# Optimization experiments

Measured on AMD Instinct MI355X. Metric: run time of the kernel, lower is better.

The kernel has to match this reference:

```python
import jax, jax.numpy as jnp
import numpy as np

N_NODES = 50000
N_EDGES = 800000
N_FEAT = 64
N_LAYERS = 3


def setup_inputs() -> dict:
    key = jax.random.key(0)
    k1, k2, k3 = jax.random.split(key, 3)
    x = jax.random.normal(k1, (N_NODES, N_FEAT), dtype=jnp.float32)
    edge_index = jax.random.randint(k2, (2, N_EDGES), 0, N_NODES, dtype=jnp.int64)
    # num_layers Linear(F, F, bias=False) weights; torch init U(-1/sqrt(F), 1/sqrt(F))
    bound = 1.0 / np.sqrt(N_FEAT)
    weights = jax.random.uniform(k3, (N_LAYERS, N_FEAT, N_FEAT), dtype=jnp.float32,
                                 minval=-bound, maxval=bound)
    return {"x": x, "edge_index": edge_index, "weights": weights}


def reference(x, edge_index, weights):
    n = x.shape[0]
    # self_loop=True: add_self_loops appends (i, i) for every node
    self_idx = jnp.arange(n, dtype=edge_index.dtype)
    src = jnp.concatenate([edge_index[0], self_idx])
    dst = jnp.concatenate([edge_index[1], self_idx])
    # in-degree for mean aggregation (>=1 thanks to self loops)
    deg = jax.ops.segment_sum(jnp.ones(src.shape[0], dtype=x.dtype), dst,
                              num_segments=n)
    inv_deg = (1.0 / jnp.maximum(deg, 1.0))[:, None]  # [N,1]
    for l in range(weights.shape[0]):
        # scatter-mean: gather source features, sum at target, divide by degree
        agg = jax.ops.segment_sum(x[src], dst, num_segments=n) * inv_deg  # [N,F]
        # Linear(bias=False): agg @ W.T
        x = agg @ weights[l].T
    return x
```

## Files before the change

### kernel.cpp

```cpp
#include <hip/hip_runtime.h>

#define NN 50000
#define NE 800000
#define NF 64
#define NL 3

typedef unsigned int uint;
typedef unsigned short ushort;
using short8 = __attribute__((ext_vector_type(8))) short;
using f32x4  = __attribute__((ext_vector_type(4))) float;

__device__ inline ushort f2bf(float f) {
    uint u = __float_as_uint(f);
    u += 0x7fffu + ((u >> 16) & 1u);
    return (ushort)(u >> 16);
}
__device__ inline float bf2f(ushort h) { return __uint_as_float(((uint)h) << 16); }


__global__ void zero_k(int* __restrict__ p, int n) {
    int i = blockIdx.x * blockDim.x + threadIdx.x;
    if (i < n) p[i] = 0;
}

__global__ void fill_k(const int* __restrict__ src, const int* __restrict__ dst,
                       int* __restrict__ deg, int* __restrict__ colp, int e) {
    int i = blockIdx.x * blockDim.x + threadIdx.x;
    if (i < e) {
        int d = dst[i];
        int slot = atomicAdd(&deg[d], 1);
        if (slot < 64) colp[(size_t)d * 64 + slot] = src[i];
    }
}

__global__ __launch_bounds__(256) void gather_k(const float* __restrict__ x,
                                                const int* __restrict__ deg,
                                                const int* __restrict__ colp,
                                                float* __restrict__ agg, int n) {
    int tid = threadIdx.x;
    int lane = tid & 63;
    int row = blockIdx.x * 4 + (tid >> 6);
    if (row >= n) return;
    int dg = deg[row];
    float invd = 1.0f / (float)(dg + 1);
    const int* cp = colp + (size_t)row * 64;
    float acc0 = x[(size_t)row * NF + lane];
    float acc1 = 0.f, acc2 = 0.f, acc3 = 0.f;
    int e = 0;
    for (; e + 8 <= dg; e += 8) {
        int4 ca = ((const int4*)cp)[(e >> 2)];
        int4 cb = ((const int4*)cp)[(e >> 2) + 1];
        float v0 = x[(size_t)ca.x * NF + lane];
        float v1 = x[(size_t)ca.y * NF + lane];
        float v2 = x[(size_t)ca.z * NF + lane];
        float v3 = x[(size_t)ca.w * NF + lane];
        float v4 = x[(size_t)cb.x * NF + lane];
        float v5 = x[(size_t)cb.y * NF + lane];
        float v6 = x[(size_t)cb.z * NF + lane];
        float v7 = x[(size_t)cb.w * NF + lane];
        acc0 += v0; acc1 += v1; acc2 += v2; acc3 += v3;
        acc0 += v4; acc1 += v5; acc2 += v6; acc3 += v7;
    }
    for (; e < dg; ++e)
        acc0 += x[(size_t)cp[e] * NF + lane];
    agg[(size_t)row * NF + lane] = (acc0 + acc1 + acc2 + acc3) * invd;
}

__global__ __launch_bounds__(256) void gemm_k(const float* __restrict__ A,
                                              const float* __restrict__ Wg,
                                              float* __restrict__ O, int n) {
    int tid = threadIdx.x;
    int lane = tid & 63, w = tid >> 6;
    int m = lane & 15, g = lane >> 4;
    int ko = g * 8;
    int row0 = blockIdx.x * 64;

    int arow = row0 + w * 16 + m;
    if (arow > n - 1) arow = n - 1;
    const float* ar = A + (size_t)arow * NF;

    float af[16];
    *(float4*)(af + 0)  = *(const float4*)(ar + ko);
    *(float4*)(af + 4)  = *(const float4*)(ar + ko + 4);
    *(float4*)(af + 8)  = *(const float4*)(ar + 32 + ko);
    *(float4*)(af + 12) = *(const float4*)(ar + 32 + ko + 4);

    short8 ah0, al0, ah1, al1;
    #pragma unroll
    for (int i = 0; i < 8; ++i) {
        ushort h = f2bf(af[i]);
        ah0[i] = (short)h; al0[i] = (short)f2bf(af[i] - bf2f(h));
        ushort h2 = f2bf(af[8 + i]);
        ah1[i] = (short)h2; al1[i] = (short)f2bf(af[8 + i] - bf2f(h2));
    }

    f32x4 acc[4];
    #pragma unroll
    for (int t = 0; t < 4; ++t) {
        const float* wr = Wg + (size_t)(t * 16 + m) * NF;
        float wf[16];
        *(float4*)(wf + 0)  = *(const float4*)(wr + ko);
        *(float4*)(wf + 4)  = *(const float4*)(wr + ko + 4);
        *(float4*)(wf + 8)  = *(const float4*)(wr + 32 + ko);
        *(float4*)(wf + 12) = *(const float4*)(wr + 32 + ko + 4);
        short8 bh0, bl0, bh1, bl1;
        #pragma unroll
        for (int i = 0; i < 8; ++i) {
            ushort h = f2bf(wf[i]);
            bh0[i] = (short)h; bl0[i] = (short)f2bf(wf[i] - bf2f(h));
            ushort h2 = f2bf(wf[8 + i]);
            bh1[i] = (short)h2; bl1[i] = (short)f2bf(wf[8 + i] - bf2f(h2));
        }
        f32x4 c = {0.f, 0.f, 0.f, 0.f};
        c = __builtin_amdgcn_mfma_f32_16x16x32_bf16(ah0, bh0, c, 0, 0, 0);
        c = __builtin_amdgcn_mfma_f32_16x16x32_bf16(ah1, bh1, c, 0, 0, 0);
        c = __builtin_amdgcn_mfma_f32_16x16x32_bf16(al0, bh0, c, 0, 0, 0);
        c = __builtin_amdgcn_mfma_f32_16x16x32_bf16(al1, bh1, c, 0, 0, 0);
        c = __builtin_amdgcn_mfma_f32_16x16x32_bf16(ah0, bl0, c, 0, 0, 0);
        c = __builtin_amdgcn_mfma_f32_16x16x32_bf16(ah1, bl1, c, 0, 0, 0);
        acc[t] = c;
    }

    #pragma unroll
    for (int t = 0; t < 4; ++t) {
        #pragma unroll
        for (int r = 0; r < 4; ++r) {
            int orow = row0 + w * 16 + g * 4 + r;
            if (orow < n) O[(size_t)orow * NF + t * 16 + m] = acc[t][r];
        }
    }
}

extern "C" void kernel_launch(void* const* d_in, const int* in_sizes, int n_in,
                              void* d_out, int out_size, void* d_ws, size_t ws_size,
                              hipStream_t stream) {
    const float* x_in = (const float*)d_in[0];
    const int*   edge = (const int*)d_in[1];
    const float* Wg   = (const float*)d_in[2];
    float* out = (float*)d_out;

    int*   deg  = (int*)d_ws;
    int*   colp = (int*)((char*)d_ws + (256 << 10));
    float* agg  = (float*)((char*)d_ws + (14 << 20));

    zero_k<<<(NN + 255) / 256, 256, 0, stream>>>(deg, NN);
    fill_k<<<(NE + 255) / 256, 256, 0, stream>>>(edge, edge + NE, deg, colp, NE);

    const int gb = (NN + 3) / 4;
    const int mb = (NN + 63) / 64;

    gather_k<<<gb, 256, 0, stream>>>(x_in, deg, colp, agg, NN);
    gemm_k  <<<mb, 256, 0, stream>>>(agg, Wg + 0 * NF * NF, out, NN);
    gather_k<<<gb, 256, 0, stream>>>(out, deg, colp, agg, NN);
    gemm_k  <<<mb, 256, 0, stream>>>(agg, Wg + 1 * NF * NF, out, NN);
    gather_k<<<gb, 256, 0, stream>>>(out, deg, colp, agg, NN);
    gemm_k  <<<mb, 256, 0, stream>>>(agg, Wg + 2 * NF * NF, out, NN);
}
```

Measured before the change: 268.6 us.

## Fuse neighbor gather with MFMA linear per layer and slice CSR fill by destination

Gather-mean and the split-bf16 MFMA linear are merged into one kernel per layer. Each block aggregates 64 rows into shared memory and multiplies them by W directly, so the agg array never goes out to global memory and back, and three launches are dropped. The fill kernel now partitions destinations into 8 slices per block group, aiming for more local atomics and colp writes. The costs are that every edge is re-read 8 times, and each block now gathers 64 rows with only 4 waves and 64-row blocks, which may reduce the latency hiding in the gather.

Result: slower. 320.9 us (+19.5%).

```diff
diff --git a/kernel.cpp b/kernel.cpp
--- a/kernel.cpp
+++ b/kernel.cpp
@@ -4,6 +4,9 @@
 #define NE 800000
 #define NF 64
 #define NL 3
+#define PAD 64
+#define NSLICE 8
+#define SLICE_N ((NN + NSLICE - 1) / NSLICE)
 
 typedef unsigned int uint;
 typedef unsigned short ushort;
@@ -17,67 +20,73 @@
 }
 __device__ inline float bf2f(ushort h) { return __uint_as_float(((uint)h) << 16); }
 
-
 __global__ void zero_k(int* __restrict__ p, int n) {
     int i = blockIdx.x * blockDim.x + threadIdx.x;
     if (i < n) p[i] = 0;
 }
 
-__global__ void fill_k(const int* __restrict__ src, const int* __restrict__ dst,
-                       int* __restrict__ deg, int* __restrict__ colp, int e) {
-    int i = blockIdx.x * blockDim.x + threadIdx.x;
-    if (i < e) {
+__global__ void fill_sliced_k(const int* __restrict__ src, const int* __restrict__ dst,
+                              int* __restrict__ deg, int* __restrict__ colp, int e) {
+    int slice = blockIdx.x & (NSLICE - 1);
+    int chunk = blockIdx.x >> 3;
+    int nch   = gridDim.x >> 3;
+    int lo = slice * SLICE_N, hi = lo + SLICE_N;
+    for (int i = chunk * blockDim.x + threadIdx.x; i < e; i += nch * blockDim.x) {
         int d = dst[i];
-        int slot = atomicAdd(&deg[d], 1);
-        if (slot < 64) colp[(size_t)d * 64 + slot] = src[i];
+        if (d >= lo && d < hi) {
+            int slot = atomicAdd(&deg[d], 1);
+            if (slot < PAD) colp[(size_t)d * PAD + slot] = src[i];
+        }
     }
 }
 
-__global__ __launch_bounds__(256) void gather_k(const float* __restrict__ x,
-                                                const int* __restrict__ deg,
-                                                const int* __restrict__ colp,
-                                                float* __restrict__ agg, int n) {
-    int tid = threadIdx.x;
-    int lane = tid & 63;
-    int row = blockIdx.x * 4 + (tid >> 6);
-    if (row >= n) return;
-    int dg = deg[row];
-    float invd = 1.0f / (float)(dg + 1);
-    const int* cp = colp + (size_t)row * 64;
-    float acc0 = x[(size_t)row * NF + lane];
-    float acc1 = 0.f, acc2 = 0.f, acc3 = 0.f;
-    int e = 0;
-    for (; e + 8 <= dg; e += 8) {
-        int4 ca = ((const int4*)cp)[(e >> 2)];
-        int4 cb = ((const int4*)cp)[(e >> 2) + 1];
-        float v0 = x[(size_t)ca.x * NF + lane];
-        float v1 = x[(size_t)ca.y * NF + lane];
-        float v2 = x[(size_t)ca.z * NF + lane];
-        float v3 = x[(size_t)ca.w * NF + lane];
-        float v4 = x[(size_t)cb.x * NF + lane];
-        float v5 = x[(size_t)cb.y * NF + lane];
-        float v6 = x[(size_t)cb.z * NF + lane];
-        float v7 = x[(size_t)cb.w * NF + lane];
-        acc0 += v0; acc1 += v1; acc2 += v2; acc3 += v3;
-        acc0 += v4; acc1 += v5; acc2 += v6; acc3 += v7;
-    }
-    for (; e < dg; ++e)
-        acc0 += x[(size_t)cp[e] * NF + lane];
-    agg[(size_t)row * NF + lane] = (acc0 + acc1 + acc2 + acc3) * invd;
-}
-
-__global__ __launch_bounds__(256) void gemm_k(const float* __restrict__ A,
-                                              const float* __restrict__ Wg,
-                                              float* __restrict__ O, int n) {
+__global__ __launch_bounds__(256) void layer_fused_k(const float* __restrict__ x,
+                                                     const int* __restrict__ deg,
+                                                     const int* __restrict__ colp,
+                                                     const float* __restrict__ Wg,
+                                                     float* __restrict__ O, int n) {
+    __shared__ float As[64][NF + 4];
     int tid = threadIdx.x;
     int lane = tid & 63, w = tid >> 6;
+    int row0 = blockIdx.x * 64;
+
+    #pragma unroll
+    for (int rr = 0; rr < 16; ++rr) {
+        int r = w * 16 + rr;
+        int row = row0 + r;
+        float val = 0.0f;
+        if (row < n) {
+            int dg = deg[row];
+            if (dg > PAD) dg = PAD;
+            const int* cp = colp + (size_t)row * PAD;
+            float acc0 = x[(size_t)row * NF + lane];
+            float acc1 = 0.f, acc2 = 0.f, acc3 = 0.f;
+            int e = 0;
+            for (; e + 8 <= dg; e += 8) {
+                int4 ca = ((const int4*)cp)[(e >> 2)];
+                int4 cb = ((const int4*)cp)[(e >> 2) + 1];
+                float v0 = x[(size_t)ca.x * NF + lane];
+                float v1 = x[(size_t)ca.y * NF + lane];
+                float v2 = x[(size_t)ca.z * NF + lane];
+                float v3 = x[(size_t)ca.w * NF + lane];
+                float v4 = x[(size_t)cb.x * NF + lane];
+                float v5 = x[(size_t)cb.y * NF + lane];
+                float v6 = x[(size_t)cb.z * NF + lane];
+                float v7 = x[(size_t)cb.w * NF + lane];
+                acc0 += v0; acc1 += v1; acc2 += v2; acc3 += v3;
+                acc0 += v4; acc1 += v5; acc2 += v6; acc3 += v7;
+            }
+            for (; e < dg; ++e)
+                acc0 += x[(size_t)cp[e] * NF + lane];
+            val = (acc0 + acc1 + acc2 + acc3) * (1.0f / (float)(dg + 1));
+        }
+        As[r][lane] = val;
+    }
+    __syncthreads();
+
     int m = lane & 15, g = lane >> 4;
     int ko = g * 8;
-    int row0 = blockIdx.x * 64;
-
-    int arow = row0 + w * 16 + m;
-    if (arow > n - 1) arow = n - 1;
-    const float* ar = A + (size_t)arow * NF;
+    const float* ar = &As[w * 16 + m][0];
 
     float af[16];
     *(float4*)(af + 0)  = *(const float4*)(ar + ko);
@@ -141,18 +150,13 @@
 
     int*   deg  = (int*)d_ws;
     int*   colp = (int*)((char*)d_ws + (256 << 10));
-    float* agg  = (float*)((char*)d_ws + (14 << 20));
+    float* bufA = (float*)((char*)d_ws + (14 << 20));
 
     zero_k<<<(NN + 255) / 256, 256, 0, stream>>>(deg, NN);
-    fill_k<<<(NE + 255) / 256, 256, 0, stream>>>(edge, edge + NE, deg, colp, NE);
+    fill_sliced_k<<<256 * NSLICE, 256, 0, stream>>>(edge, edge + NE, deg, colp, NE);
 
-    const int gb = (NN + 3) / 4;
-    const int mb = (NN + 63) / 64;
-
-    gather_k<<<gb, 256, 0, stream>>>(x_in, deg, colp, agg, NN);
-    gemm_k  <<<mb, 256, 0, stream>>>(agg, Wg + 0 * NF * NF, out, NN);
-    gather_k<<<gb, 256, 0, stream>>>(out, deg, colp, agg, NN);
-    gemm_k  <<<mb, 256, 0, stream>>>(agg, Wg + 1 * NF * NF, out, NN);
-    gather_k<<<gb, 256, 0, stream>>>(out, deg, colp, agg, NN);
-    gemm_k  <<<mb, 256, 0, stream>>>(agg, Wg + 2 * NF * NF, out, NN);
+    const int lb = (NN + 63) / 64;
+    layer_fused_k<<<lb, 256, 0, stream>>>(x_in, deg, colp, Wg + 0 * NF * NF, out,  NN);
+    layer_fused_k<<<lb, 256, 0, stream>>>(out,  deg, colp, Wg + 1 * NF * NF, bufA, NN);
+    layer_fused_k<<<lb, 256, 0, stream>>>(bufA, deg, colp, Wg + 2 * NF * NF, out,  NN);
 }
```

## Fold three layer weights into one matrix and run a single GEMM

Applied to the files above, without the earlier changes.

Because mean aggregation is linear and commutes with a right-multiplication by a weight matrix, the three per-layer GEMMs are replaced by one GEMM with the precombined matrix W3·W2·W1, computed once in a small single-block kernel. The three gathers now run back-to-back on raw features, followed by one GEMM in place. The gather inner loop is unrolled to 16 edges with a 4-edge remainder loop, and the degree is clamped to the padded capacity. Floating-point summation order changes, and the final GEMM reads and writes the same buffer.

Measured after the change: 250.0 us. 1.07x faster.

```diff
diff --git a/kernel.cpp b/kernel.cpp
--- a/kernel.cpp
+++ b/kernel.cpp
@@ -4,6 +4,7 @@
 #define NE 800000
 #define NF 64
 #define NL 3
+#define PAD 64
 
 typedef unsigned int uint;
 typedef unsigned short ushort;
@@ -16,7 +17,6 @@
     return (ushort)(u >> 16);
 }
 __device__ inline float bf2f(ushort h) { return __uint_as_float(((uint)h) << 16); }
-
 
 __global__ void zero_k(int* __restrict__ p, int n) {
     int i = blockIdx.x * blockDim.x + threadIdx.x;
@@ -29,7 +29,35 @@
     if (i < e) {
         int d = dst[i];
         int slot = atomicAdd(&deg[d], 1);
-        if (slot < 64) colp[(size_t)d * 64 + slot] = src[i];
+        if (slot < PAD) colp[(size_t)d * PAD + slot] = src[i];
+    }
+}
+
+__global__ __launch_bounds__(256) void wcomb_k(const float* __restrict__ Wg,
+                                               float* __restrict__ Wc) {
+    __shared__ float s1[64][65], s2[64][65], st[64][65];
+    int tid = threadIdx.x;
+    for (int i = tid; i < 64 * 64; i += 256) {
+        s1[i >> 6][i & 63] = Wg[i];
+        s2[i >> 6][i & 63] = Wg[4096 + i];
+    }
+    __syncthreads();
+    for (int i = tid; i < 64 * 64; i += 256) {
+        int a = i >> 6, c = i & 63;
+        float s = 0.f;
+        #pragma unroll
+        for (int b = 0; b < 64; ++b) s = fmaf(s2[a][b], s1[b][c], s);
+        st[a][c] = s;
+    }
+    __syncthreads();
+    for (int i = tid; i < 64 * 64; i += 256) s1[i >> 6][i & 63] = Wg[8192 + i];
+    __syncthreads();
+    for (int i = tid; i < 64 * 64; i += 256) {
+        int o = i >> 6, c = i & 63;
+        float s = 0.f;
+        #pragma unroll
+        for (int a = 0; a < 64; ++a) s = fmaf(s1[o][a], st[a][c], s);
+        Wc[i] = s;
     }
 }
 
@@ -42,27 +70,46 @@
     int row = blockIdx.x * 4 + (tid >> 6);
     if (row >= n) return;
     int dg = deg[row];
+    if (dg > PAD) dg = PAD;
     float invd = 1.0f / (float)(dg + 1);
-    const int* cp = colp + (size_t)row * 64;
+    const int4* cp4 = (const int4*)(colp + (size_t)row * PAD);
     float acc0 = x[(size_t)row * NF + lane];
     float acc1 = 0.f, acc2 = 0.f, acc3 = 0.f;
     int e = 0;
-    for (; e + 8 <= dg; e += 8) {
-        int4 ca = ((const int4*)cp)[(e >> 2)];
-        int4 cb = ((const int4*)cp)[(e >> 2) + 1];
-        float v0 = x[(size_t)ca.x * NF + lane];
-        float v1 = x[(size_t)ca.y * NF + lane];
-        float v2 = x[(size_t)ca.z * NF + lane];
-        float v3 = x[(size_t)ca.w * NF + lane];
-        float v4 = x[(size_t)cb.x * NF + lane];
-        float v5 = x[(size_t)cb.y * NF + lane];
-        float v6 = x[(size_t)cb.z * NF + lane];
-        float v7 = x[(size_t)cb.w * NF + lane];
+    for (; e + 16 <= dg; e += 16) {
+        int4 ia = cp4[(e >> 2) + 0];
+        int4 ib = cp4[(e >> 2) + 1];
+        int4 ic = cp4[(e >> 2) + 2];
+        int4 id = cp4[(e >> 2) + 3];
+        float v0  = x[(size_t)ia.x * NF + lane];
+        float v1  = x[(size_t)ia.y * NF + lane];
+        float v2  = x[(size_t)ia.z * NF + lane];
+        float v3  = x[(size_t)ia.w * NF + lane];
+        float v4  = x[(size_t)ib.x * NF + lane];
+        float v5  = x[(size_t)ib.y * NF + lane];
+        float v6  = x[(size_t)ib.z * NF + lane];
+        float v7  = x[(size_t)ib.w * NF + lane];
+        float v8  = x[(size_t)ic.x * NF + lane];
+        float v9  = x[(size_t)ic.y * NF + lane];
+        float v10 = x[(size_t)ic.z * NF + lane];
+        float v11 = x[(size_t)ic.w * NF + lane];
+        float v12 = x[(size_t)id.x * NF + lane];
+        float v13 = x[(size_t)id.y * NF + lane];
+        float v14 = x[(size_t)id.z * NF + lane];
+        float v15 = x[(size_t)id.w * NF + lane];
+        acc0 += v0 + v4;  acc1 += v1 + v5;  acc2 += v2 + v6;  acc3 += v3 + v7;
+        acc0 += v8 + v12; acc1 += v9 + v13; acc2 += v10 + v14; acc3 += v11 + v15;
+    }
+    for (; e + 4 <= dg; e += 4) {
+        int4 ia = cp4[e >> 2];
+        float v0 = x[(size_t)ia.x * NF + lane];
+        float v1 = x[(size_t)ia.y * NF + lane];
+        float v2 = x[(size_t)ia.z * NF + lane];
+        float v3 = x[(size_t)ia.w * NF + lane];
         acc0 += v0; acc1 += v1; acc2 += v2; acc3 += v3;
-        acc0 += v4; acc1 += v5; acc2 += v6; acc3 += v7;
     }
     for (; e < dg; ++e)
-        acc0 += x[(size_t)cp[e] * NF + lane];
+        acc0 += x[(size_t)colp[(size_t)row * PAD + e] * NF + lane];
     agg[(size_t)row * NF + lane] = (acc0 + acc1 + acc2 + acc3) * invd;
 }
 
@@ -140,19 +187,19 @@
     float* out = (float*)d_out;
 
     int*   deg  = (int*)d_ws;
+    float* Wc   = (float*)((char*)d_ws + (208 << 10));
     int*   colp = (int*)((char*)d_ws + (256 << 10));
-    float* agg  = (float*)((char*)d_ws + (14 << 20));
-
-    zero_k<<<(NN + 255) / 256, 256, 0, stream>>>(deg, NN);
-    fill_k<<<(NE + 255) / 256, 256, 0, stream>>>(edge, edge + NE, deg, colp, NE);
+    float* bufA = (float*)((char*)d_ws + (14 << 20));
+
+    zero_k <<<(NN + 255) / 256, 256, 0, stream>>>(deg, NN);
+    fill_k <<<(NE + 255) / 256, 256, 0, stream>>>(edge, edge + NE, deg, colp, NE);
+    wcomb_k<<<1, 256, 0, stream>>>(Wg, Wc);
 
     const int gb = (NN + 3) / 4;
     const int mb = (NN + 63) / 64;
 
-    gather_k<<<gb, 256, 0, stream>>>(x_in, deg, colp, agg, NN);
-    gemm_k  <<<mb, 256, 0, stream>>>(agg, Wg + 0 * NF * NF, out, NN);
-    gather_k<<<gb, 256, 0, stream>>>(out, deg, colp, agg, NN);
-    gemm_k  <<<mb, 256, 0, stream>>>(agg, Wg + 1 * NF * NF, out, NN);
-    gather_k<<<gb, 256, 0, stream>>>(out, deg, colp, agg, NN);
-    gemm_k  <<<mb, 256, 0, stream>>>(agg, Wg + 2 * NF * NF, out, NN);
-}
+    gather_k<<<gb, 256, 0, stream>>>(x_in, deg, colp, out,  NN);
+    gather_k<<<gb, 256, 0, stream>>>(out,  deg, colp, bufA, NN);
+    gather_k<<<gb, 256, 0, stream>>>(bufA, deg, colp, out,  NN);
+    gemm_k  <<<mb, 256, 0, stream>>>(out, Wc, out, NN);
+}
```
